# Performance work log

Measured on AMD Instinct MI355X. Metric: run time of the kernel, lower is better.

Reference implementation:

```python
import jax, jax.numpy as jnp
import numpy as np


def _ste_round(x):
    # straight-through-estimator round (matches brevitas RoundSte)
    return x + jax.lax.stop_gradient(jnp.round(x) - x)


def _fake_quant(x, bits):
    # symmetric per-tensor fake quantization with max-abs scaling
    qmax = 2.0 ** (bits - 1) - 1.0  # 127 for int8, 7 for int4
    s = jnp.max(jnp.abs(x)) / qmax
    q = jnp.clip(_ste_round(x / s), -qmax, qmax)
    return q * s, s


def setup_inputs() -> dict:
    key = jax.random.key(0)
    k1, k2, k3 = jax.random.split(key, 3)
    B, S, D, H = 8, 2048, 4096, 4096  # tokens = B*S
    x = jax.random.normal(k1, (B * S, D), dtype=jnp.float32)
    W = jax.random.normal(k2, (H, D), dtype=jnp.float32) * (1.0 / np.sqrt(D))
    b = jax.random.normal(k3, (H,), dtype=jnp.float32) * 0.01
    return {"x": x, "W": W, "b": b}


def reference(x, W, b):
    # inputQuant (Int8ActPerTensorFloat) applied twice back-to-back is
    # idempotent in effect; linear1 input_quant re-quantizes the int8 tensor.
    xq, s_in = _fake_quant(x, 8)          # int8 activation quant
    Wq, s_w = _fake_quant(W, 4)           # 4-bit weight quant (weight_bit_width=4)
    s_b = s_in * s_w                      # Int32Bias: scale = input_scale * weight_scale
    bmax = 2.0 ** 31 - 1.0
    bq = jnp.clip(_ste_round(b / s_b), -bmax, bmax) * s_b
    y = xq @ Wq.T + bq                    # quantized matmul (dequantized math)
    yq, _ = _fake_quant(y, 8)             # output_quant Int8ActPerTensorFloat
    return yq
```

## Files before the change

### kernel.cpp

```cpp
#include <hip/hip_runtime.h>
#include <stdint.h>


typedef __attribute__((ext_vector_type(4))) int i32x4;

#define BM 256
#define BN 256
#define BKB 128

__device__ __forceinline__ void async_copy16(const void* g, void* l) {
  __builtin_amdgcn_global_load_lds((const __attribute__((address_space(1))) void*)g,
                                   (__attribute__((address_space(3))) void*)l,
                                   16, 0, 0);
}

__device__ __forceinline__ float wave_max64(float v) {
#pragma unroll
  for (int off = 32; off > 0; off >>= 1) v = fmaxf(v, __shfl_xor(v, off, 64));
  return v;
}

__device__ __forceinline__ float max4(float4 v) {
  return fmaxf(fmaxf(fabsf(v.x), fabsf(v.y)), fmaxf(fabsf(v.z), fabsf(v.w)));
}

#define WBLK 1024
__global__ void maxabs_both(const float4* __restrict__ x, int n4x,
                            const float4* __restrict__ w, int n4w,
                            unsigned* __restrict__ scal) {
  const bool isW = (int)blockIdx.x < WBLK;
  const float4* __restrict__ p = isW ? w : x;
  const int n4 = isW ? n4w : n4x;
  const int bid = isW ? blockIdx.x : blockIdx.x - WBLK;
  const int nb = isW ? WBLK : gridDim.x - WBLK;
  const int stride = nb * blockDim.x;

  float m0 = 0.f, m1 = 0.f, m2 = 0.f, m3 = 0.f;
  int i = bid * blockDim.x + threadIdx.x;
  for (; i + 3 * stride < n4; i += 4 * stride) {
    m0 = fmaxf(m0, max4(p[i]));
    m1 = fmaxf(m1, max4(p[i + stride]));
    m2 = fmaxf(m2, max4(p[i + 2 * stride]));
    m3 = fmaxf(m3, max4(p[i + 3 * stride]));
  }
  for (; i < n4; i += stride) m0 = fmaxf(m0, max4(p[i]));
  float m = wave_max64(fmaxf(fmaxf(m0, m1), fmaxf(m2, m3)));

  __shared__ float wm[4];
  if ((threadIdx.x & 63) == 0) wm[threadIdx.x >> 6] = m;
  __syncthreads();
  if (threadIdx.x == 0)
    atomicMax(&scal[isW ? 1 : 0],
              __float_as_uint(fmaxf(fmaxf(wm[0], wm[1]), fmaxf(wm[2], wm[3]))));
}

__device__ __forceinline__ unsigned pack4(float4 v, float inv, float qmax) {
  unsigned b0 = (unsigned)(int)fminf(fmaxf(rintf(v.x * inv), -qmax), qmax) & 0xffu;
  unsigned b1 = (unsigned)(int)fminf(fmaxf(rintf(v.y * inv), -qmax), qmax) & 0xffu;
  unsigned b2 = (unsigned)(int)fminf(fmaxf(rintf(v.z * inv), -qmax), qmax) & 0xffu;
  unsigned b3 = (unsigned)(int)fminf(fmaxf(rintf(v.w * inv), -qmax), qmax) & 0xffu;
  return b0 | (b1 << 8) | (b2 << 16) | (b3 << 24);
}

__global__ void quant_both(const float4* __restrict__ x, unsigned* __restrict__ xq, int n4x,
                           const float4* __restrict__ w, unsigned* __restrict__ wq, int n4w,
                           const unsigned* __restrict__ scal) {
  const bool isW = (int)blockIdx.x < WBLK;
  const float4* __restrict__ src = isW ? w : x;
  unsigned* __restrict__ dst = isW ? wq : xq;
  const int n4 = isW ? n4w : n4x;
  const int bid = isW ? blockIdx.x : blockIdx.x - WBLK;
  const int nb = isW ? WBLK : gridDim.x - WBLK;
  const float qmax = isW ? 7.f : 127.f;
  const float inv = qmax / __uint_as_float(scal[isW ? 1 : 0]);
  const int stride = nb * blockDim.x;

  int i = bid * blockDim.x + threadIdx.x;
  for (; i + stride < n4; i += 2 * stride) {
    float4 a = src[i];
    float4 b = src[i + stride];
    dst[i] = pack4(a, inv, qmax);
    dst[i + stride] = pack4(b, inv, qmax);
  }
  if (i < n4) dst[i] = pack4(src[i], inv, qmax);
}

__device__ __forceinline__ void stage_tile(const uint8_t* __restrict__ Aq,
                                           const uint8_t* __restrict__ Bq,
                                           uint8_t* sa, uint8_t* sb,
                                           int t, int K, int bm, int bn, int k0) {
#pragma unroll
  for (int j = 0; j < 4; ++j) {
    const int id = j * 512 + t;
    const int r = id >> 3;
    const int cc = id & 7;
    const int gc = (cc ^ (r & 7)) << 4;
    async_copy16(Aq + (size_t)(bm + r) * K + k0 + gc, sa + id * 16);
  }
#pragma unroll
  for (int j = 0; j < 4; ++j) {
    const int id = j * 512 + t;
    const int r = id >> 3;
    const int cc = id & 7;
    const int gc = (cc ^ (r & 7)) << 4;
    async_copy16(Bq + (size_t)(bn + r) * K + k0 + gc, sb + id * 16);
  }
}

__global__ __launch_bounds__(512, 2) void gemm_i8(
    const uint8_t* __restrict__ Aq, const uint8_t* __restrict__ Bq,
    const float* __restrict__ bias, float* __restrict__ Out,
    unsigned* __restrict__ scal, int M, int N, int K) {
  __shared__ uint8_t sA[2][BM * BKB];
  __shared__ uint8_t sB[2][BN * BKB];
  __shared__ float wred[8];

  const int t = threadIdx.x;
  const int lane = t & 63, wave = t >> 6;
  const int wm = wave >> 2, wn = wave & 3;
  const int quad = lane >> 4, l16 = lane & 15;

  const int nwg = (int)gridDim.x;
  const int wg = ((int)blockIdx.x & 7) * (nwg >> 3) + ((int)blockIdx.x >> 3);
  const int nbx = N / BN;
  const int bm = (wg / nbx) * BM, bn = (wg % nbx) * BN;

  i32x4 acc[8][4] = {};
  const int NT = K >> 7;

  stage_tile(Aq, Bq, sA[0], sB[0], t, K, bm, bn, 0);

  for (int tt = 0; tt < NT; ++tt) {
    const int cur = tt & 1;
    if (tt + 1 < NT) {
      stage_tile(Aq, Bq, sA[cur ^ 1], sB[cur ^ 1], t, K, bm, bn, (tt + 1) << 7);
      asm volatile("s_waitcnt vmcnt(8)" ::: "memory");
    } else {
      asm volatile("s_waitcnt vmcnt(0)" ::: "memory");
    }
    asm volatile("s_barrier" ::: "memory");

    const uint8_t* sa = sA[cur];
    const uint8_t* sb = sB[cur];
#pragma unroll
    for (int kk = 0; kk < 2; ++kk) {
      i32x4 bf[4];
#pragma unroll
      for (int nt = 0; nt < 4; ++nt) {
        const int row = wn * 64 + nt * 16 + l16;
        const int p = (quad + kk * 4) ^ (row & 7);
        bf[nt] = *(const i32x4*)&sb[row * BKB + p * 16];
      }
#pragma unroll
      for (int mh = 0; mh < 2; ++mh) {
        i32x4 af[4];
#pragma unroll
        for (int mt = 0; mt < 4; ++mt) {
          const int row = wm * 128 + mh * 64 + mt * 16 + l16;
          const int p = (quad + kk * 4) ^ (row & 7);
          af[mt] = *(const i32x4*)&sa[row * BKB + p * 16];
        }
        asm volatile("s_barrier" ::: "memory");
        __builtin_amdgcn_s_setprio(1);
#pragma unroll
        for (int mt = 0; mt < 4; ++mt)
#pragma unroll
          for (int nt = 0; nt < 4; ++nt)
            acc[mh * 4 + mt][nt] = __builtin_amdgcn_mfma_i32_16x16x64_i8(
                af[mt], bf[nt], acc[mh * 4 + mt][nt], 0, 0, 0);
        __builtin_amdgcn_s_setprio(0);
        asm volatile("s_barrier" ::: "memory");
      }
    }
  }

  const float s_in = __uint_as_float(scal[0]) / 127.0f;
  const float s_w = __uint_as_float(scal[1]) / 7.0f;
  const float s_b = s_in * s_w;
  float bi[4];
#pragma unroll
  for (int nt = 0; nt < 4; ++nt) {
    const int n = bn + wn * 64 + nt * 16 + l16;
    bi[nt] = rintf(bias[n] / s_b);
  }
  float lmax = 0.f;
#pragma unroll
  for (int a = 0; a < 8; ++a) {
#pragma unroll
    for (int r = 0; r < 4; ++r) {
      const int m = bm + wm * 128 + a * 16 + quad * 4 + r;
      float* orow = Out + (size_t)m * N + bn + wn * 64 + l16;
#pragma unroll
      for (int nt = 0; nt < 4; ++nt) {
        float tv = (float)acc[a][nt][r] + bi[nt];
        orow[nt * 16] = tv;
        lmax = fmaxf(lmax, fabsf(tv));
      }
    }
  }
  lmax = wave_max64(lmax);
  if (lane == 0) wred[wave] = lmax;
  __syncthreads();
  if (t == 0) {
    float m = wred[0];
#pragma unroll
    for (int i = 1; i < 8; ++i) m = fmaxf(m, wred[i]);
    atomicMax(&scal[2], __float_as_uint(m));
  }
}

__device__ __forceinline__ float4 quantize4(float4 v, float inv, float s_out) {
  v.x = fminf(fmaxf(rintf(v.x * inv), -127.f), 127.f) * s_out;
  v.y = fminf(fmaxf(rintf(v.y * inv), -127.f), 127.f) * s_out;
  v.z = fminf(fmaxf(rintf(v.z * inv), -127.f), 127.f) * s_out;
  v.w = fminf(fmaxf(rintf(v.w * inv), -127.f), 127.f) * s_out;
  return v;
}

__global__ void finalize4(float4* __restrict__ out, int n4, const unsigned* __restrict__ scal) {
  const float s_in = __uint_as_float(scal[0]) / 127.0f;
  const float s_w = __uint_as_float(scal[1]) / 7.0f;
  const float s_b = s_in * s_w;
  const float maxt = __uint_as_float(scal[2]);
  const float s_out = (s_b * maxt) / 127.0f;
  const float inv = 127.0f / maxt;
  const int stride = gridDim.x * blockDim.x;
  int i = blockIdx.x * blockDim.x + threadIdx.x;
  for (; i + stride < n4; i += 2 * stride) {
    float4 a = out[i];
    float4 b = out[i + stride];
    out[i] = quantize4(a, inv, s_out);
    out[i + stride] = quantize4(b, inv, s_out);
  }
  if (i < n4) out[i] = quantize4(out[i], inv, s_out);
}

extern "C" void kernel_launch(void* const* d_in, const int* in_sizes, int n_in,
                              void* d_out, int out_size, void* d_ws, size_t ws_size,
                              hipStream_t stream) {
  const float* x = (const float*)d_in[0];
  const float* W = (const float*)d_in[1];
  const float* b = (const float*)d_in[2];
  float* out = (float*)d_out;

  const int N = in_sizes[2];
  const int K = in_sizes[1] / N;
  const int M = in_sizes[0] / K;

  unsigned* scal = (unsigned*)d_ws;
  const size_t OFF = 4096;
  uint8_t* xq = (uint8_t*)d_ws + OFF;
  uint8_t* wq = xq + (size_t)M * K;

  const int n4x = (M / 4) * K;
  const int n4w = (N / 4) * K;

  hipMemsetAsync(scal, 0, 16, stream);
  maxabs_both<<<WBLK + 4096, 256, 0, stream>>>((const float4*)x, n4x,
                                               (const float4*)W, n4w, scal);
  quant_both<<<WBLK + 4096, 256, 0, stream>>>((const float4*)x, (unsigned*)xq, n4x,
                                              (const float4*)W, (unsigned*)wq, n4w, scal);

  const int nblk = (M / BM) * (N / BN);
  gemm_i8<<<nblk, 512, 0, stream>>>(xq, wq, b, out, scal, M, N, K);

  finalize4<<<8192, 256, 0, stream>>>((float4*)out, (int)((size_t)M * N / 4), scal);
}
```

Baseline: 1.003 ms.

## Switch GEMM mainloop to triple-buffered BK=64 pipeline with interleaved staging

```diff
diff --git a/kernel.cpp b/kernel.cpp
--- a/kernel.cpp
+++ b/kernel.cpp
@@ -6,7 +6,7 @@
 
 #define BM 256
 #define BN 256
-#define BKB 128
+#define BKB 64
 
 __device__ __forceinline__ void async_copy16(const void* g, void* l) {
   __builtin_amdgcn_global_load_lds((const __attribute__((address_space(1))) void*)g,
@@ -85,34 +85,33 @@
   if (i < n4) dst[i] = pack4(src[i], inv, qmax);
 }
 
-__device__ __forceinline__ void stage_tile(const uint8_t* __restrict__ Aq,
-                                           const uint8_t* __restrict__ Bq,
-                                           uint8_t* sa, uint8_t* sb,
-                                           int t, int K, int bm, int bn, int k0) {
-#pragma unroll
-  for (int j = 0; j < 4; ++j) {
+__device__ __forceinline__ void stage_mat(const uint8_t* __restrict__ src,
+                                          uint8_t* dst, int t, int K,
+                                          int brow, int k0) {
+#pragma unroll
+  for (int j = 0; j < 2; ++j) {
     const int id = j * 512 + t;
-    const int r = id >> 3;
-    const int cc = id & 7;
-    const int gc = (cc ^ (r & 7)) << 4;
-    async_copy16(Aq + (size_t)(bm + r) * K + k0 + gc, sa + id * 16);
-  }
-#pragma unroll
-  for (int j = 0; j < 4; ++j) {
-    const int id = j * 512 + t;
-    const int r = id >> 3;
-    const int cc = id & 7;
-    const int gc = (cc ^ (r & 7)) << 4;
-    async_copy16(Bq + (size_t)(bn + r) * K + k0 + gc, sb + id * 16);
-  }
+    const int L = id >> 3;
+    const int pl = id & 7;
+    const int cl = pl ^ (L & 7);
+    const int r = L * 2 + (cl >> 2);
+    const int c = cl & 3;
+    async_copy16(src + (size_t)(brow + r) * K + k0 + c * 16, dst + id * 16);
+  }
+}
+
+__device__ __forceinline__ const i32x4* frag_ptr(const uint8_t* base, int row, int quad) {
+  const int L = row >> 1;
+  const int p = (((row & 1) << 2) | quad) ^ (L & 7);
+  return (const i32x4*)(base + L * 128 + p * 16);
 }
 
 __global__ __launch_bounds__(512, 2) void gemm_i8(
     const uint8_t* __restrict__ Aq, const uint8_t* __restrict__ Bq,
     const float* __restrict__ bias, float* __restrict__ Out,
     unsigned* __restrict__ scal, int M, int N, int K) {
-  __shared__ uint8_t sA[2][BM * BKB];
-  __shared__ uint8_t sB[2][BN * BKB];
+  __shared__ uint8_t sA[3][BM * BKB];
+  __shared__ uint8_t sB[3][BN * BKB];
   __shared__ float wred[8];
 
   const int t = threadIdx.x;
@@ -126,52 +125,59 @@
   const int bm = (wg / nbx) * BM, bn = (wg % nbx) * BN;
 
   i32x4 acc[8][4] = {};
-  const int NT = K >> 7;
-
-  stage_tile(Aq, Bq, sA[0], sB[0], t, K, bm, bn, 0);
+  const int NT = K >> 6;
+
+  stage_mat(Aq, sA[0], t, K, bm, 0);
+  stage_mat(Bq, sB[0], t, K, bn, 0);
+  stage_mat(Aq, sA[1], t, K, bm, BKB);
+  stage_mat(Bq, sB[1], t, K, bn, BKB);
+  asm volatile("s_waitcnt vmcnt(4)" ::: "memory");
+  asm volatile("s_barrier" ::: "memory");
 
   for (int tt = 0; tt < NT; ++tt) {
-    const int cur = tt & 1;
-    if (tt + 1 < NT) {
-      stage_tile(Aq, Bq, sA[cur ^ 1], sB[cur ^ 1], t, K, bm, bn, (tt + 1) << 7);
-      asm volatile("s_waitcnt vmcnt(8)" ::: "memory");
-    } else {
+    const int cur = tt % 3;
+    const int nxt = (tt + 2) % 3;
+    const uint8_t* sa = sA[cur];
+    const uint8_t* sb = sB[cur];
+    const bool pf = (tt + 2) < NT;
+
+    i32x4 bf[4], af[4];
+#pragma unroll
+    for (int nt = 0; nt < 4; ++nt)
+      bf[nt] = *frag_ptr(sb, wn * 64 + nt * 16 + l16, quad);
+#pragma unroll
+    for (int mt = 0; mt < 4; ++mt)
+      af[mt] = *frag_ptr(sa, wm * 128 + mt * 16 + l16, quad);
+    if (pf) stage_mat(Aq, sA[nxt], t, K, bm, (tt + 2) << 6);
+    asm volatile("s_barrier" ::: "memory");
+    __builtin_amdgcn_s_setprio(1);
+#pragma unroll
+    for (int mt = 0; mt < 4; ++mt)
+#pragma unroll
+      for (int nt = 0; nt < 4; ++nt)
+        acc[mt][nt] = __builtin_amdgcn_mfma_i32_16x16x64_i8(af[mt], bf[nt], acc[mt][nt], 0, 0, 0);
+    __builtin_amdgcn_s_setprio(0);
+    asm volatile("s_barrier" ::: "memory");
+
+    i32x4 ag[4];
+#pragma unroll
+    for (int mt = 0; mt < 4; ++mt)
+      ag[mt] = *frag_ptr(sa, wm * 128 + 64 + mt * 16 + l16, quad);
+    if (pf) stage_mat(Bq, sB[nxt], t, K, bn, (tt + 2) << 6);
+    asm volatile("s_barrier" ::: "memory");
+    __builtin_amdgcn_s_setprio(1);
+#pragma unroll
+    for (int mt = 0; mt < 4; ++mt)
+#pragma unroll
+      for (int nt = 0; nt < 4; ++nt)
+        acc[4 + mt][nt] = __builtin_amdgcn_mfma_i32_16x16x64_i8(ag[mt], bf[nt], acc[4 + mt][nt], 0, 0, 0);
+    __builtin_amdgcn_s_setprio(0);
+    if (pf) {
+      asm volatile("s_waitcnt vmcnt(4)" ::: "memory");
+    } else if (tt + 1 < NT) {
       asm volatile("s_waitcnt vmcnt(0)" ::: "memory");
     }
     asm volatile("s_barrier" ::: "memory");
-
-    const uint8_t* sa = sA[cur];
-    const uint8_t* sb = sB[cur];
-#pragma unroll
-    for (int kk = 0; kk < 2; ++kk) {
-      i32x4 bf[4];
-#pragma unroll
-      for (int nt = 0; nt < 4; ++nt) {
-        const int row = wn * 64 + nt * 16 + l16;
-        const int p = (quad + kk * 4) ^ (row & 7);
-        bf[nt] = *(const i32x4*)&sb[row * BKB + p * 16];
-      }
-#pragma unroll
-      for (int mh = 0; mh < 2; ++mh) {
-        i32x4 af[4];
-#pragma unroll
-        for (int mt = 0; mt < 4; ++mt) {
-          const int row = wm * 128 + mh * 64 + mt * 16 + l16;
-          const int p = (quad + kk * 4) ^ (row & 7);
-          af[mt] = *(const i32x4*)&sa[row * BKB + p * 16];
-        }
-        asm volatile("s_barrier" ::: "memory");
-        __builtin_amdgcn_s_setprio(1);
-#pragma unroll
-        for (int mt = 0; mt < 4; ++mt)
-#pragma unroll
-          for (int nt = 0; nt < 4; ++nt)
-            acc[mh * 4 + mt][nt] = __builtin_amdgcn_mfma_i32_16x16x64_i8(
-                af[mt], bf[nt], acc[mh * 4 + mt][nt], 0, 0, 0);
-        __builtin_amdgcn_s_setprio(0);
-        asm volatile("s_barrier" ::: "memory");
-      }
-    }
   }
 
   const float s_in = __uint_as_float(scal[0]) / 127.0f;
```

After: 943.3 us. 1.06x faster.
